# Performance work log

Hardware: AMD Instinct MI355X
Metric: run time of the kernel (lower is better)

Reference implementation:

```python
import jax, jax.numpy as jnp
import numpy as np

H = 16
D_IN = 1024
D_OUT = 1024
D_K = D_OUT // H
B = 8
S = 1024


def setup_inputs() -> dict:
    key = jax.random.key(0)
    ks = jax.random.split(key, 9)
    scale = 1.0 / np.sqrt(D_IN)
    inp = {
        "query": jax.random.normal(ks[0], (B, S, D_IN), dtype=jnp.float32),
        "key_": jax.random.normal(ks[1], (B, S, D_IN), dtype=jnp.float32),
        "value": jax.random.normal(ks[2], (B, S, D_IN), dtype=jnp.float32),
        "Wq": jax.random.uniform(ks[3], (D_OUT, D_IN), jnp.float32, -scale, scale),
        "bq": jax.random.uniform(ks[4], (D_OUT,), jnp.float32, -scale, scale),
        "Wk": jax.random.uniform(ks[5], (D_OUT, D_IN), jnp.float32, -scale, scale),
        "bk": jax.random.uniform(ks[6], (D_OUT,), jnp.float32, -scale, scale),
        "Wv": jax.random.uniform(ks[7], (D_OUT, D_IN), jnp.float32, -scale, scale),
        "bv": jax.random.uniform(ks[8], (D_OUT,), jnp.float32, -scale, scale),
    }
    return inp


def reference(query, key_, value, Wq, bq, Wk, bk, Wv, bv):
    batch = query.shape[0]

    def proj(x, W, b):
        # torch Linear: x @ W.T + b, then view(B, -1, h, d_k).transpose(1, 2)
        y = jnp.einsum("bsd,od->bso", x, W) + b
        return y.reshape(batch, -1, H, D_K).transpose(0, 2, 1, 3)  # [B, h, S, d_k]

    q = proj(query, Wq, bq)
    k = proj(key_, Wk, bk)
    v = proj(value, Wv, bv)

    scores = jnp.einsum("bhqd,bhkd->bhqk", q, k) / (D_K ** 0.5)  # [B, h, S, S]
    attn = jax.nn.softmax(scores, axis=-1)
    x = jnp.einsum("bhqk,bhkd->bhqd", attn, v)  # [B, h, S, d_k]

    # transpose(1, 2).contiguous().view(batch, -1) -> flatten seq*d_out
    return x.transpose(0, 2, 1, 3).reshape(batch, -1)
```

## Files before the change

### kernel.cpp

```cpp
#include <hip/hip_runtime.h>
#include <math.h>

#define NH   16
#define DK   64
#define SEQL 1024
#define NB   8
#define DIN  1024
#define PSTR 76

typedef __bf16 bf16;
typedef __attribute__((ext_vector_type(8))) __bf16 bf16x8;
typedef __attribute__((ext_vector_type(4))) __bf16 bf16x4;
typedef __attribute__((ext_vector_type(4))) float f32x4;

#define QSCALE 0.18033688011112042f

static __device__ __forceinline__ f32x4 mfma_bf16(bf16x8 a, bf16x8 b, f32x4 c) {
  return __builtin_amdgcn_mfma_f32_16x16x32_bf16(a, b, c, 0, 0, 0);
}

static __device__ __forceinline__ void async16(const bf16* g, bf16* l) {
  __builtin_amdgcn_global_load_lds(
      (const __attribute__((address_space(1))) void*)g,
      (__attribute__((address_space(3))) void*)l, 16, 0, 0);
}

__global__ __launch_bounds__(256)
void cvt6_kernel(const float* __restrict__ s0, const float* __restrict__ s1,
                 const float* __restrict__ s2, const float* __restrict__ s3,
                 const float* __restrict__ s4, const float* __restrict__ s5,
                 bf16* __restrict__ d0, bf16* __restrict__ d1,
                 bf16* __restrict__ d2, bf16* __restrict__ d3,
                 bf16* __restrict__ d4, bf16* __restrict__ d5,
                 int n8a, int n8b) {
  const int y = blockIdx.y;
  const int n8 = (y < 3) ? n8a : n8b;
  const int i = blockIdx.x * 256 + threadIdx.x;
  if (i >= n8) return;
  const float* s = (y == 0) ? s0 : (y == 1) ? s1 : (y == 2) ? s2
                 : (y == 3) ? s3 : (y == 4) ? s4 : s5;
  bf16* d = (y == 0) ? d0 : (y == 1) ? d1 : (y == 2) ? d2
          : (y == 3) ? d3 : (y == 4) ? d4 : d5;
  const f32x4* sp = (const f32x4*)s;
  const f32x4 a = sp[2 * i], b = sp[2 * i + 1];
  bf16x8 r;
  r[0] = (bf16)a[0]; r[1] = (bf16)a[1]; r[2] = (bf16)a[2]; r[3] = (bf16)a[3];
  r[4] = (bf16)b[0]; r[5] = (bf16)b[1]; r[6] = (bf16)b[2]; r[7] = (bf16)b[3];
  ((bf16x8*)d)[i] = r;
}

__global__ __launch_bounds__(256, 2)
void proj_kernel(const bf16* __restrict__ Xq, const bf16* __restrict__ Xk,
                 const bf16* __restrict__ Xv,
                 const bf16* __restrict__ Wq, const bf16* __restrict__ Wk,
                 const bf16* __restrict__ Wv,
                 const float* __restrict__ Bq, const float* __restrict__ Bk,
                 const float* __restrict__ Bv,
                 bf16* __restrict__ Yq, bf16* __restrict__ Yk,
                 bf16* __restrict__ Yv) {
  const int z = blockIdx.z;
  const bf16*  X  = (z == 0) ? Xq : (z == 1) ? Xk : Xv;
  const bf16*  W  = (z == 0) ? Wq : (z == 1) ? Wk : Wv;
  const float* Bi = (z == 0) ? Bq : (z == 1) ? Bk : Bv;
  bf16*        Y  = (z == 0) ? Yq : (z == 1) ? Yk : Yv;

  const int m0 = blockIdx.x * 128;
  const int n0 = blockIdx.y * 128;

  __shared__ __attribute__((aligned(16))) bf16 As[128 * 32];
  __shared__ __attribute__((aligned(16))) bf16 Bs[128 * 32];

  const int t    = threadIdx.x;
  const int l    = t & 63;
  const int w    = t >> 6;
  const int l15  = l & 15;
  const int quad = l >> 4;
  const int wm   = w & 1;
  const int wn   = w >> 1;

  f32x4 acc[4][4];
#pragma unroll
  for (int i = 0; i < 4; ++i)
#pragma unroll
    for (int j = 0; j < 4; ++j) acc[i][j] = (f32x4){0.f, 0.f, 0.f, 0.f};

  const int srow   = l >> 2;
  const int gchunk = (l & 3) ^ ((l >> 3) & 3);

  for (int k0 = 0; k0 < DIN; k0 += 32) {
    __syncthreads();
#pragma unroll
    for (int i = 0; i < 2; ++i) {
      const int slab = w * 32 + i * 16;
      const int r    = slab + srow;
      async16(X + (size_t)(m0 + r) * DIN + k0 + gchunk * 8, As + slab * 32);
      async16(W + (size_t)(n0 + r) * DIN + k0 + gchunk * 8, Bs + slab * 32);
    }
    __syncthreads();

    bf16x8 af[4], bfr[4];
    const int swz = quad ^ ((l15 >> 1) & 3);
#pragma unroll
    for (int mi = 0; mi < 4; ++mi)
      af[mi] = *(const bf16x8*)(As + (wm * 64 + mi * 16 + l15) * 32 + swz * 8);
#pragma unroll
    for (int nj = 0; nj < 4; ++nj)
      bfr[nj] = *(const bf16x8*)(Bs + (wn * 64 + nj * 16 + l15) * 32 + swz * 8);
#pragma unroll
    for (int mi = 0; mi < 4; ++mi)
#pragma unroll
      for (int nj = 0; nj < 4; ++nj)
        acc[mi][nj] = mfma_bf16(af[mi], bfr[nj], acc[mi][nj]);
  }

  if (z == 2) {
#pragma unroll
    for (int nj = 0; nj < 4; ++nj) {
      const int o    = n0 + wn * 64 + nj * 16 + l15;
      const float bv = Bi[o];
      const int h    = o >> 6;
      const int d    = o & 63;
#pragma unroll
      for (int mi = 0; mi < 4; ++mi) {
        const int m  = m0 + wm * 64 + mi * 16 + quad * 4;
        const int bl = m >> 10;
        const int s  = m & (SEQL - 1);
        bf16x4 pk;
#pragma unroll
        for (int r = 0; r < 4; ++r) pk[r] = (bf16)(acc[mi][nj][r] + bv);
        *(bf16x4*)(Y + ((size_t)(bl * NH + h) * DK + d) * SEQL + s) = pk;
      }
    }
  } else {
    const float scale = (z == 0) ? QSCALE : 1.0f;
#pragma unroll
    for (int nj = 0; nj < 4; ++nj) {
      const int o    = n0 + wn * 64 + nj * 16 + l15;
      const float bv = Bi[o];
      const int h    = o >> 6;
      const int d    = o & 63;
#pragma unroll
      for (int mi = 0; mi < 4; ++mi) {
#pragma unroll
        for (int r = 0; r < 4; ++r) {
          const int m  = m0 + wm * 64 + mi * 16 + quad * 4 + r;
          const int bl = m >> 10;
          const int s  = m & (SEQL - 1);
          Y[(size_t)(((bl * NH + h) << 10) | s) * DK + d] =
              (bf16)((acc[mi][nj][r] + bv) * scale);
        }
      }
    }
  }
}

__global__ __launch_bounds__(256, 2)
void attn_kernel(const bf16* __restrict__ Q, const bf16* __restrict__ K,
                 const bf16* __restrict__ V, float* __restrict__ Out, int b0) {
  const int bhl = blockIdx.x;
  const int q0  = blockIdx.y * 256;
  const int bg  = b0 + (bhl >> 4);
  const int h   = bhl & 15;
  const int t    = threadIdx.x;
  const int l    = t & 63;
  const int w    = t >> 6;
  const int l15  = l & 15;
  const int quad = l >> 4;

  const bf16* Qh = Q + (size_t)bhl * SEQL * DK;
  const bf16* Kh = K + (size_t)bhl * SEQL * DK;
  const bf16* Vh = V + (size_t)bhl * DK * SEQL;

  __shared__ __attribute__((aligned(16))) bf16 sKs[2][64 * 64];
  __shared__ __attribute__((aligned(16))) bf16 sVt[2][64 * 64];
  __shared__ __attribute__((aligned(16))) bf16 sPl[4][4][16 * PSTR];

  bf16x8 qf[4][2];
#pragma unroll
  for (int g = 0; g < 4; ++g)
#pragma unroll
    for (int hh = 0; hh < 2; ++hh)
      qf[g][hh] = *(const bf16x8*)(Qh + (size_t)(q0 + w * 64 + g * 16 + l15) * DK +
                                   hh * 32 + quad * 8);

  bf16x8 ones;
#pragma unroll
  for (int j = 0; j < 8; ++j) ones[j] = (bf16)1.0f;

  f32x4 oacc[4][4];
#pragma unroll
  for (int g = 0; g < 4; ++g)
#pragma unroll
    for (int n = 0; n < 4; ++n) oacc[g][n] = (f32x4){0.f, 0.f, 0.f, 0.f};
  f32x4 sacc[4];
#pragma unroll
  for (int g = 0; g < 4; ++g) sacc[g] = (f32x4){0.f, 0.f, 0.f, 0.f};

  const int drow   = l >> 3;
  const int dchunk = l & 7;

#define STAGE_KV(T, BB)                                                      \
  {                                                                          \
    const int kbs = (T) * 64;                                                \
    _Pragma("unroll")                                                        \
    for (int i = 0; i < 2; ++i) {                                            \
      const int r = w * 16 + i * 8 + drow;                                   \
      async16(Kh + (size_t)(kbs + r) * DK + (dchunk ^ (r & 7)) * 8,          \
              &sKs[BB][(w * 16 + i * 8) * 64]);                              \
      async16(Vh + (size_t)r * SEQL + kbs + (dchunk ^ (r & 7)) * 8,          \
              &sVt[BB][(w * 16 + i * 8) * 64]);                              \
    }                                                                        \
  }

  const int NT = SEQL / 64;

  STAGE_KV(0, 0)
  STAGE_KV(1, 1)
  asm volatile("s_waitcnt vmcnt(4)" ::: "memory");
  __builtin_amdgcn_s_barrier();

  for (int tt = 0; tt < NT; ++tt) {
    const int bb = tt & 1;

    bf16x8 kf[4][2];
#pragma unroll
    for (int c = 0; c < 4; ++c)
#pragma unroll
      for (int hh = 0; hh < 2; ++hh)
        kf[c][hh] = *(const bf16x8*)(&sKs[bb][(c * 16 + l15) * 64 +
                                     (((hh * 4 + quad) ^ (l15 & 7)) * 8)]);
    bf16x8 vfr[4][2];
#pragma unroll
    for (int n = 0; n < 4; ++n)
#pragma unroll
      for (int hh = 0; hh < 2; ++hh)
        vfr[n][hh] = *(const bf16x8*)(&sVt[bb][(n * 16 + l15) * 64 +
                                      (((hh * 4 + quad) ^ (l15 & 7)) * 8)]);

    asm volatile("s_waitcnt lgkmcnt(0)" ::: "memory");
    __builtin_amdgcn_sched_barrier(0);
    __builtin_amdgcn_s_barrier();
    if (tt + 2 < NT) STAGE_KV(tt + 2, bb)
    __builtin_amdgcn_sched_barrier(0);

#pragma unroll
    for (int g = 0; g < 4; ++g) {
#pragma unroll
      for (int c = 0; c < 4; ++c) {
        f32x4 cs = (f32x4){0.f, 0.f, 0.f, 0.f};
        cs = mfma_bf16(kf[c][0], qf[g][0], cs);
        cs = mfma_bf16(kf[c][1], qf[g][1], cs);
        bf16x4 pk;
#pragma unroll
        for (int r = 0; r < 4; ++r) pk[r] = (bf16)exp2f(cs[r]);
        *(bf16x4*)(&sPl[w][g][l15 * PSTR + c * 16 + quad * 4]) = pk;
      }
    }

#pragma unroll
    for (int g = 0; g < 4; ++g) {
      const bf16x8 pf0 = *(const bf16x8*)(&sPl[w][g][l15 * PSTR + quad * 8]);
      const bf16x8 pf1 = *(const bf16x8*)(&sPl[w][g][l15 * PSTR + 32 + quad * 8]);
#pragma unroll
      for (int n = 0; n < 4; ++n) {
        oacc[g][n] = mfma_bf16(pf0, vfr[n][0], oacc[g][n]);
        oacc[g][n] = mfma_bf16(pf1, vfr[n][1], oacc[g][n]);
      }
      sacc[g] = mfma_bf16(pf0, ones, sacc[g]);
      sacc[g] = mfma_bf16(pf1, ones, sacc[g]);
    }

    if (tt + 2 < NT) {
      asm volatile("s_waitcnt vmcnt(4)" ::: "memory");
    } else if (tt + 2 == NT) {
      asm volatile("s_waitcnt vmcnt(0)" ::: "memory");
    }
    if (tt + 1 < NT) __builtin_amdgcn_s_barrier();
  }
#undef STAGE_KV

#pragma unroll
  for (int g = 0; g < 4; ++g) {
    float linv[4];
#pragma unroll
    for (int r = 0; r < 4; ++r) linv[r] = 1.0f / sacc[g][r];
#pragma unroll
    for (int n = 0; n < 4; ++n) {
      const int d = n * 16 + l15;
#pragma unroll
      for (int r = 0; r < 4; ++r) {
        const int qrow = q0 + w * 64 + g * 16 + quad * 4 + r;
        Out[(size_t)((bg * SEQL + qrow) * NH + h) * DK + d] =
            oacc[g][n][r] * linv[r];
      }
    }
  }
}

extern "C" void kernel_launch(void* const* d_in, const int* in_sizes, int n_in,
                              void* d_out, int out_size, void* d_ws,
                              size_t ws_size, hipStream_t stream) {
  const float* q  = (const float*)d_in[0];
  const float* k  = (const float*)d_in[1];
  const float* v  = (const float*)d_in[2];
  const float* Wq = (const float*)d_in[3];
  const float* bq = (const float*)d_in[4];
  const float* Wk = (const float*)d_in[5];
  const float* bk = (const float*)d_in[6];
  const float* Wv = (const float*)d_in[7];
  const float* bv = (const float*)d_in[8];
  float* out = (float*)d_out;

  const size_t wElems = (size_t)DIN * DIN;
  const size_t wBytes = 3 * wElems * sizeof(bf16);
  const size_t perBatch = 6 * (size_t)SEQL * DIN * sizeof(bf16);
  int nbg = (ws_size > wBytes) ? (int)((ws_size - wBytes) / perBatch) : 1;
  if (nbg < 1) nbg = 1;
  if (nbg > NB) nbg = NB;

  bf16* Wqb = (bf16*)d_ws;
  bf16* Wkb = Wqb + wElems;
  bf16* Wvb = Wkb + wElems;
  const size_t g1 = (size_t)nbg * SEQL * DIN;
  bf16* Xqb = Wvb + wElems;
  bf16* Xkb = Xqb + g1;
  bf16* Xvb = Xkb + g1;
  bf16* Yqb = Xvb + g1;
  bf16* Ykb = Yqb + g1;
  bf16* Yvb = Ykb + g1;

  const int w8 = (int)(wElems / 8);

  for (int b0 = 0; b0 < NB; b0 += nbg) {
    const int nb = (NB - b0 < nbg) ? (NB - b0) : nbg;
    const int n8 = nb * SEQL * DIN / 8;
    const size_t xoff = (size_t)b0 * SEQL * DIN;
    const int xb = (n8 + 255) / 256;
    const int wb = (w8 + 255) / 256;
    dim3 gX((xb > wb) ? xb : wb, 6);
    cvt6_kernel<<<gX, 256, 0, stream>>>(q + xoff, k + xoff, v + xoff,
                                        Wq, Wk, Wv,
                                        Xqb, Xkb, Xvb, Wqb, Wkb, Wvb,
                                        n8, w8);

    dim3 gP(nb * 8, 8, 3);
    proj_kernel<<<gP, 256, 0, stream>>>(Xqb, Xkb, Xvb, Wqb, Wkb, Wvb,
                                        bq, bk, bv, Yqb, Ykb, Yvb);

    dim3 gA(nb * NH, SEQL / 256);
    attn_kernel<<<gA, 256, 0, stream>>>(Yqb, Ykb, Yvb, out, b0);
  }
}
```

Measured before the change: 279.7 us.

## Halve attention query tile, raise occupancy, and vectorize Q/K projection stores

The attention kernel now gives each block 128 query rows instead of 256 (32 per wave). It launches twice as many blocks with a launch-bounds target of 4 blocks per CU. V fragments are read from LDS on demand, and the barrier plus next K/V prefetch move to the end of each iteration, which lowers register pressure but shortens the load/compute overlap. In the projection kernel, the Q/K paths swap MFMA operand roles so each lane holds contiguous d elements and can write bf16x4 vector stores instead of scattered scalar stores, at the cost of more K/V reloads per query.

```diff
diff --git a/kernel.cpp b/kernel.cpp
--- a/kernel.cpp
+++ b/kernel.cpp
@@ -78,6 +78,11 @@
   const int wm   = w & 1;
   const int wn   = w >> 1;
 
+  const bf16* Atile = (z == 2) ? As : Bs;
+  const bf16* Btile = (z == 2) ? Bs : As;
+  const int arow0 = ((z == 2) ? wm : wn) * 64;
+  const int brow0 = ((z == 2) ? wn : wm) * 64;
+
   f32x4 acc[4][4];
 #pragma unroll
   for (int i = 0; i < 4; ++i)
@@ -102,10 +107,10 @@
     const int swz = quad ^ ((l15 >> 1) & 3);
 #pragma unroll
     for (int mi = 0; mi < 4; ++mi)
-      af[mi] = *(const bf16x8*)(As + (wm * 64 + mi * 16 + l15) * 32 + swz * 8);
+      af[mi] = *(const bf16x8*)(Atile + (arow0 + mi * 16 + l15) * 32 + swz * 8);
 #pragma unroll
     for (int nj = 0; nj < 4; ++nj)
-      bfr[nj] = *(const bf16x8*)(Bs + (wn * 64 + nj * 16 + l15) * 32 + swz * 8);
+      bfr[nj] = *(const bf16x8*)(Btile + (brow0 + nj * 16 + l15) * 32 + swz * 8);
 #pragma unroll
     for (int mi = 0; mi < 4; ++mi)
 #pragma unroll
@@ -133,32 +138,31 @@
     }
   } else {
     const float scale = (z == 0) ? QSCALE : 1.0f;
-#pragma unroll
-    for (int nj = 0; nj < 4; ++nj) {
-      const int o    = n0 + wn * 64 + nj * 16 + l15;
-      const float bv = Bi[o];
-      const int h    = o >> 6;
-      const int d    = o & 63;
-#pragma unroll
-      for (int mi = 0; mi < 4; ++mi) {
-#pragma unroll
-        for (int r = 0; r < 4; ++r) {
-          const int m  = m0 + wm * 64 + mi * 16 + quad * 4 + r;
-          const int bl = m >> 10;
-          const int s  = m & (SEQL - 1);
-          Y[(size_t)(((bl * NH + h) << 10) | s) * DK + d] =
-              (bf16)((acc[mi][nj][r] + bv) * scale);
-        }
-      }
-    }
-  }
-}
-
-__global__ __launch_bounds__(256, 2)
+    const int hq = (n0 + wn * 64) >> 6;
+#pragma unroll
+    for (int mi = 0; mi < 4; ++mi) {
+      const int dbase = mi * 16 + quad * 4;
+      const f32x4 bv4 = *(const f32x4*)(Bi + n0 + wn * 64 + dbase);
+#pragma unroll
+      for (int nj = 0; nj < 4; ++nj) {
+        const int m  = m0 + wm * 64 + nj * 16 + l15;
+        const int bl = m >> 10;
+        const int s  = m & (SEQL - 1);
+        bf16x4 pk;
+#pragma unroll
+        for (int r = 0; r < 4; ++r)
+          pk[r] = (bf16)((acc[mi][nj][r] + bv4[r]) * scale);
+        *(bf16x4*)(Y + (size_t)(((bl * NH + hq) << 10) | s) * DK + dbase) = pk;
+      }
+    }
+  }
+}
+
+__global__ __launch_bounds__(256, 4)
 void attn_kernel(const bf16* __restrict__ Q, const bf16* __restrict__ K,
                  const bf16* __restrict__ V, float* __restrict__ Out, int b0) {
   const int bhl = blockIdx.x;
-  const int q0  = blockIdx.y * 256;
+  const int q0  = blockIdx.y * 128;
   const int bg  = b0 + (bhl >> 4);
   const int h   = bhl & 15;
   const int t    = threadIdx.x;
@@ -173,28 +177,28 @@
 
   __shared__ __attribute__((aligned(16))) bf16 sKs[2][64 * 64];
   __shared__ __attribute__((aligned(16))) bf16 sVt[2][64 * 64];
-  __shared__ __attribute__((aligned(16))) bf16 sPl[4][4][16 * PSTR];
-
-  bf16x8 qf[4][2];
-#pragma unroll
-  for (int g = 0; g < 4; ++g)
+  __shared__ __attribute__((aligned(16))) bf16 sPl[4][2][16 * PSTR];
+
+  bf16x8 qf[2][2];
+#pragma unroll
+  for (int g = 0; g < 2; ++g)
 #pragma unroll
     for (int hh = 0; hh < 2; ++hh)
-      qf[g][hh] = *(const bf16x8*)(Qh + (size_t)(q0 + w * 64 + g * 16 + l15) * DK +
+      qf[g][hh] = *(const bf16x8*)(Qh + (size_t)(q0 + w * 32 + g * 16 + l15) * DK +
                                    hh * 32 + quad * 8);
 
   bf16x8 ones;
 #pragma unroll
   for (int j = 0; j < 8; ++j) ones[j] = (bf16)1.0f;
 
-  f32x4 oacc[4][4];
-#pragma unroll
-  for (int g = 0; g < 4; ++g)
+  f32x4 oacc[2][4];
+#pragma unroll
+  for (int g = 0; g < 2; ++g)
 #pragma unroll
     for (int n = 0; n < 4; ++n) oacc[g][n] = (f32x4){0.f, 0.f, 0.f, 0.f};
-  f32x4 sacc[4];
-#pragma unroll
-  for (int g = 0; g < 4; ++g) sacc[g] = (f32x4){0.f, 0.f, 0.f, 0.f};
+  f32x4 sacc[2];
+  sacc[0] = (f32x4){0.f, 0.f, 0.f, 0.f};
+  sacc[1] = (f32x4){0.f, 0.f, 0.f, 0.f};
 
   const int drow   = l >> 3;
   const int dchunk = l & 7;
@@ -229,22 +233,9 @@
       for (int hh = 0; hh < 2; ++hh)
         kf[c][hh] = *(const bf16x8*)(&sKs[bb][(c * 16 + l15) * 64 +
                                      (((hh * 4 + quad) ^ (l15 & 7)) * 8)]);
-    bf16x8 vfr[4][2];
-#pragma unroll
-    for (int n = 0; n < 4; ++n)
-#pragma unroll
-      for (int hh = 0; hh < 2; ++hh)
-        vfr[n][hh] = *(const bf16x8*)(&sVt[bb][(n * 16 + l15) * 64 +
-                                      (((hh * 4 + quad) ^ (l15 & 7)) * 8)]);
-
-    asm volatile("s_waitcnt lgkmcnt(0)" ::: "memory");
-    __builtin_amdgcn_sched_barrier(0);
-    __builtin_amdgcn_s_barrier();
-    if (tt + 2 < NT) STAGE_KV(tt + 2, bb)
-    __builtin_amdgcn_sched_barrier(0);
-
-#pragma unroll
-    for (int g = 0; g < 4; ++g) {
+
+#pragma unroll
+    for (int g = 0; g < 2; ++g) {
 #pragma unroll
       for (int c = 0; c < 4; ++c) {
         f32x4 cs = (f32x4){0.f, 0.f, 0.f, 0.f};
@@ -257,20 +248,36 @@
       }
     }
 
-#pragma unroll
-    for (int g = 0; g < 4; ++g) {
-      const bf16x8 pf0 = *(const bf16x8*)(&sPl[w][g][l15 * PSTR + quad * 8]);
-      const bf16x8 pf1 = *(const bf16x8*)(&sPl[w][g][l15 * PSTR + 32 + quad * 8]);
-#pragma unroll
-      for (int n = 0; n < 4; ++n) {
-        oacc[g][n] = mfma_bf16(pf0, vfr[n][0], oacc[g][n]);
-        oacc[g][n] = mfma_bf16(pf1, vfr[n][1], oacc[g][n]);
-      }
-      sacc[g] = mfma_bf16(pf0, ones, sacc[g]);
-      sacc[g] = mfma_bf16(pf1, ones, sacc[g]);
-    }
-
+    bf16x8 pf[2][2];
+#pragma unroll
+    for (int g = 0; g < 2; ++g) {
+      pf[g][0] = *(const bf16x8*)(&sPl[w][g][l15 * PSTR + quad * 8]);
+      pf[g][1] = *(const bf16x8*)(&sPl[w][g][l15 * PSTR + 32 + quad * 8]);
+    }
+
+#pragma unroll
+    for (int n = 0; n < 4; ++n) {
+      const bf16x8 v0 = *(const bf16x8*)(&sVt[bb][(n * 16 + l15) * 64 +
+                                         ((quad ^ (l15 & 7)) * 8)]);
+      const bf16x8 v1 = *(const bf16x8*)(&sVt[bb][(n * 16 + l15) * 64 +
+                                         ((((4 + quad)) ^ (l15 & 7)) * 8)]);
+#pragma unroll
+      for (int g = 0; g < 2; ++g) {
+        oacc[g][n] = mfma_bf16(pf[g][0], v0, oacc[g][n]);
+        oacc[g][n] = mfma_bf16(pf[g][1], v1, oacc[g][n]);
+      }
+    }
+#pragma unroll
+    for (int g = 0; g < 2; ++g) {
+      sacc[g] = mfma_bf16(pf[g][0], ones, sacc[g]);
+      sacc[g] = mfma_bf16(pf[g][1], ones, sacc[g]);
+    }
+
+    asm volatile("s_waitcnt lgkmcnt(0)" ::: "memory");
+    __builtin_amdgcn_sched_barrier(0);
+    __builtin_amdgcn_s_barrier();
     if (tt + 2 < NT) {
+      STAGE_KV(tt + 2, bb)
       asm volatile("s_waitcnt vmcnt(4)" ::: "memory");
     } else if (tt + 2 == NT) {
       asm volatile("s_waitcnt vmcnt(0)" ::: "memory");
@@ -280,7 +287,7 @@
 #undef STAGE_KV
 
 #pragma unroll
-  for (int g = 0; g < 4; ++g) {
+  for (int g = 0; g < 2; ++g) {
     float linv[4];
 #pragma unroll
     for (int r = 0; r < 4; ++r) linv[r] = 1.0f / sacc[g][r];
@@ -289,7 +296,7 @@
       const int d = n * 16 + l15;
 #pragma unroll
       for (int r = 0; r < 4; ++r) {
-        const int qrow = q0 + w * 64 + g * 16 + quad * 4 + r;
+        const int qrow = q0 + w * 32 + g * 16 + quad * 4 + r;
         Out[(size_t)((bg * SEQL + qrow) * NH + h) * DK + d] =
             oacc[g][n][r] * linv[r];
       }
@@ -347,7 +354,7 @@
     proj_kernel<<<gP, 256, 0, stream>>>(Xqb, Xkb, Xvb, Wqb, Wkb, Wvb,
                                         bq, bk, bv, Yqb, Ykb, Yvb);
 
-    dim3 gA(nb * NH, SEQL / 256);
+    dim3 gA(nb * NH, SEQL / 128);
     attn_kernel<<<gA, 256, 0, stream>>>(Yqb, Ykb, Yvb, out, b0);
   }
 }
```

After: 293.2 us. 4.8% more time.

## Fuse activation fp32-to-bf16 conversion into projection GEMM loads

Applied to the files above, without the earlier changes.

Instead of a separate pass that converts query/key/value to bf16 in the workspace, the projection kernel now loads fp32 activations straight into shared memory with async loads and converts to bf16 while reading fragments. Only the weights are still pre-converted, in a single kernel outside the batch loop. For Q and K the MFMA operand order is swapped, so the epilogue writes contiguous bf16x4 vectors along d with vectorised bias loads instead of scalar scattered stores. This removes an extra round trip of activations through global memory, but doubles shared memory for the X tile and adds conversion work inside the GEMM loop.

```diff
diff --git a/kernel.cpp b/kernel.cpp
--- a/kernel.cpp
+++ b/kernel.cpp
@@ -19,28 +19,20 @@
   return __builtin_amdgcn_mfma_f32_16x16x32_bf16(a, b, c, 0, 0, 0);
 }
 
-static __device__ __forceinline__ void async16(const bf16* g, bf16* l) {
+static __device__ __forceinline__ void async16(const void* g, void* l) {
   __builtin_amdgcn_global_load_lds(
       (const __attribute__((address_space(1))) void*)g,
       (__attribute__((address_space(3))) void*)l, 16, 0, 0);
 }
 
 __global__ __launch_bounds__(256)
-void cvt6_kernel(const float* __restrict__ s0, const float* __restrict__ s1,
-                 const float* __restrict__ s2, const float* __restrict__ s3,
-                 const float* __restrict__ s4, const float* __restrict__ s5,
-                 bf16* __restrict__ d0, bf16* __restrict__ d1,
-                 bf16* __restrict__ d2, bf16* __restrict__ d3,
-                 bf16* __restrict__ d4, bf16* __restrict__ d5,
-                 int n8a, int n8b) {
-  const int y = blockIdx.y;
-  const int n8 = (y < 3) ? n8a : n8b;
+void cvt3_kernel(const float* __restrict__ s0, const float* __restrict__ s1,
+                 const float* __restrict__ s2, bf16* __restrict__ d0,
+                 bf16* __restrict__ d1, bf16* __restrict__ d2, int n8) {
   const int i = blockIdx.x * 256 + threadIdx.x;
   if (i >= n8) return;
-  const float* s = (y == 0) ? s0 : (y == 1) ? s1 : (y == 2) ? s2
-                 : (y == 3) ? s3 : (y == 4) ? s4 : s5;
-  bf16* d = (y == 0) ? d0 : (y == 1) ? d1 : (y == 2) ? d2
-          : (y == 3) ? d3 : (y == 4) ? d4 : d5;
+  const float* s = (blockIdx.y == 0) ? s0 : (blockIdx.y == 1) ? s1 : s2;
+  bf16*        d = (blockIdx.y == 0) ? d0 : (blockIdx.y == 1) ? d1 : d2;
   const f32x4* sp = (const f32x4*)s;
   const f32x4 a = sp[2 * i], b = sp[2 * i + 1];
   bf16x8 r;
@@ -50,8 +42,8 @@
 }
 
 __global__ __launch_bounds__(256, 2)
-void proj_kernel(const bf16* __restrict__ Xq, const bf16* __restrict__ Xk,
-                 const bf16* __restrict__ Xv,
+void proj_kernel(const float* __restrict__ Xq, const float* __restrict__ Xk,
+                 const float* __restrict__ Xv,
                  const bf16* __restrict__ Wq, const bf16* __restrict__ Wk,
                  const bf16* __restrict__ Wv,
                  const float* __restrict__ Bq, const float* __restrict__ Bk,
@@ -59,7 +51,7 @@
                  bf16* __restrict__ Yq, bf16* __restrict__ Yk,
                  bf16* __restrict__ Yv) {
   const int z = blockIdx.z;
-  const bf16*  X  = (z == 0) ? Xq : (z == 1) ? Xk : Xv;
+  const float* X  = (z == 0) ? Xq : (z == 1) ? Xk : Xv;
   const bf16*  W  = (z == 0) ? Wq : (z == 1) ? Wk : Wv;
   const float* Bi = (z == 0) ? Bq : (z == 1) ? Bk : Bv;
   bf16*        Y  = (z == 0) ? Yq : (z == 1) ? Yk : Yv;
@@ -67,8 +59,8 @@
   const int m0 = blockIdx.x * 128;
   const int n0 = blockIdx.y * 128;
 
-  __shared__ __attribute__((aligned(16))) bf16 As[128 * 32];
-  __shared__ __attribute__((aligned(16))) bf16 Bs[128 * 32];
+  __shared__ __attribute__((aligned(16))) float Xs[128 * 32];
+  __shared__ __attribute__((aligned(16))) bf16  Ws[128 * 32];
 
   const int t    = threadIdx.x;
   const int l    = t & 63;
@@ -86,6 +78,10 @@
 
   const int srow   = l >> 2;
   const int gchunk = (l & 3) ^ ((l >> 3) & 3);
+  const int xrow   = l >> 3;
+  const int xchunk = (l & 7) ^ xrow;
+
+  const int rx7 = l15 & 7;
 
   for (int k0 = 0; k0 < DIN; k0 += 32) {
     __syncthreads();
@@ -93,24 +89,43 @@
     for (int i = 0; i < 2; ++i) {
       const int slab = w * 32 + i * 16;
       const int r    = slab + srow;
-      async16(X + (size_t)(m0 + r) * DIN + k0 + gchunk * 8, As + slab * 32);
-      async16(W + (size_t)(n0 + r) * DIN + k0 + gchunk * 8, Bs + slab * 32);
+      async16(W + (size_t)(n0 + r) * DIN + k0 + gchunk * 8, Ws + slab * 32);
+    }
+#pragma unroll
+    for (int c = 0; c < 4; ++c) {
+      const int slab = w * 32 + c * 8;
+      const int r    = slab + xrow;
+      async16(X + (size_t)(m0 + r) * DIN + k0 + xchunk * 4, Xs + slab * 32);
     }
     __syncthreads();
 
-    bf16x8 af[4], bfr[4];
-    const int swz = quad ^ ((l15 >> 1) & 3);
-#pragma unroll
-    for (int mi = 0; mi < 4; ++mi)
-      af[mi] = *(const bf16x8*)(As + (wm * 64 + mi * 16 + l15) * 32 + swz * 8);
-#pragma unroll
-    for (int nj = 0; nj < 4; ++nj)
-      bfr[nj] = *(const bf16x8*)(Bs + (wn * 64 + nj * 16 + l15) * 32 + swz * 8);
-#pragma unroll
-    for (int mi = 0; mi < 4; ++mi)
-#pragma unroll
-      for (int nj = 0; nj < 4; ++nj)
-        acc[mi][nj] = mfma_bf16(af[mi], bfr[nj], acc[mi][nj]);
+    bf16x8 xf[4], wf[4];
+    const int swzW = quad ^ ((l15 >> 1) & 3);
+#pragma unroll
+    for (int i = 0; i < 4; ++i) {
+      const int xr = wm * 64 + i * 16 + l15;
+      const f32x4 lo = *(const f32x4*)(Xs + xr * 32 + (((quad << 1) | 0) ^ rx7) * 4);
+      const f32x4 hi = *(const f32x4*)(Xs + xr * 32 + (((quad << 1) | 1) ^ rx7) * 4);
+#pragma unroll
+      for (int j = 0; j < 4; ++j) {
+        xf[i][j]     = (bf16)lo[j];
+        xf[i][4 + j] = (bf16)hi[j];
+      }
+      wf[i] = *(const bf16x8*)(Ws + (wn * 64 + i * 16 + l15) * 32 + swzW * 8);
+    }
+    if (z == 2) {
+#pragma unroll
+      for (int mi = 0; mi < 4; ++mi)
+#pragma unroll
+        for (int nj = 0; nj < 4; ++nj)
+          acc[mi][nj] = mfma_bf16(xf[mi], wf[nj], acc[mi][nj]);
+    } else {
+#pragma unroll
+      for (int mi = 0; mi < 4; ++mi)
+#pragma unroll
+        for (int nj = 0; nj < 4; ++nj)
+          acc[mi][nj] = mfma_bf16(wf[mi], xf[nj], acc[mi][nj]);
+    }
   }
 
   if (z == 2) {
@@ -133,22 +148,21 @@
     }
   } else {
     const float scale = (z == 0) ? QSCALE : 1.0f;
-#pragma unroll
-    for (int nj = 0; nj < 4; ++nj) {
-      const int o    = n0 + wn * 64 + nj * 16 + l15;
-      const float bv = Bi[o];
-      const int h    = o >> 6;
-      const int d    = o & 63;
-#pragma unroll
-      for (int mi = 0; mi < 4; ++mi) {
-#pragma unroll
-        for (int r = 0; r < 4; ++r) {
-          const int m  = m0 + wm * 64 + mi * 16 + quad * 4 + r;
-          const int bl = m >> 10;
-          const int s  = m & (SEQL - 1);
-          Y[(size_t)(((bl * NH + h) << 10) | s) * DK + d] =
-              (bf16)((acc[mi][nj][r] + bv) * scale);
-        }
+    const int hq = (n0 + wn * 64) >> 6;
+#pragma unroll
+    for (int mi = 0; mi < 4; ++mi) {
+      const int dbase = mi * 16 + quad * 4;
+      const f32x4 bv4 = *(const f32x4*)(Bi + n0 + wn * 64 + dbase);
+#pragma unroll
+      for (int nj = 0; nj < 4; ++nj) {
+        const int m  = m0 + wm * 64 + nj * 16 + l15;
+        const int bl = m >> 10;
+        const int s  = m & (SEQL - 1);
+        bf16x4 pk;
+#pragma unroll
+        for (int r = 0; r < 4; ++r)
+          pk[r] = (bf16)((acc[mi][nj][r] + bv4[r]) * scale);
+        *(bf16x4*)(Y + (size_t)(((bl * NH + hq) << 10) | s) * DK + dbase) = pk;
       }
     }
   }
@@ -313,7 +327,7 @@
 
   const size_t wElems = (size_t)DIN * DIN;
   const size_t wBytes = 3 * wElems * sizeof(bf16);
-  const size_t perBatch = 6 * (size_t)SEQL * DIN * sizeof(bf16);
+  const size_t perBatch = 3 * (size_t)SEQL * DIN * sizeof(bf16);
   int nbg = (ws_size > wBytes) ? (int)((ws_size - wBytes) / perBatch) : 1;
   if (nbg < 1) nbg = 1;
   if (nbg > NB) nbg = NB;
@@ -322,29 +336,21 @@
   bf16* Wkb = Wqb + wElems;
   bf16* Wvb = Wkb + wElems;
   const size_t g1 = (size_t)nbg * SEQL * DIN;
-  bf16* Xqb = Wvb + wElems;
-  bf16* Xkb = Xqb + g1;
-  bf16* Xvb = Xkb + g1;
-  bf16* Yqb = Xvb + g1;
+  bf16* Yqb = Wvb + wElems;
   bf16* Ykb = Yqb + g1;
   bf16* Yvb = Ykb + g1;
 
   const int w8 = (int)(wElems / 8);
+  dim3 gW((w8 + 255) / 256, 3);
+  cvt3_kernel<<<gW, 256, 0, stream>>>(Wq, Wk, Wv, Wqb, Wkb, Wvb, w8);
 
   for (int b0 = 0; b0 < NB; b0 += nbg) {
     const int nb = (NB - b0 < nbg) ? (NB - b0) : nbg;
-    const int n8 = nb * SEQL * DIN / 8;
     const size_t xoff = (size_t)b0 * SEQL * DIN;
-    const int xb = (n8 + 255) / 256;
-    const int wb = (w8 + 255) / 256;
-    dim3 gX((xb > wb) ? xb : wb, 6);
-    cvt6_kernel<<<gX, 256, 0, stream>>>(q + xoff, k + xoff, v + xoff,
-                                        Wq, Wk, Wv,
-                                        Xqb, Xkb, Xvb, Wqb, Wkb, Wvb,
-                                        n8, w8);
 
     dim3 gP(nb * 8, 8, 3);
-    proj_kernel<<<gP, 256, 0, stream>>>(Xqb, Xkb, Xvb, Wqb, Wkb, Wvb,
+    proj_kernel<<<gP, 256, 0, stream>>>(q + xoff, k + xoff, v + xoff,
+                                        Wqb, Wkb, Wvb,
                                         bq, bk, bv, Yqb, Ykb, Yvb);
 
     dim3 gA(nb * NH, SEQL / 256);
```

Result: slower. 316.3 us (+13.1%).

## Double projection K-tile to 64 and transpose MFMA operands for vectorized Q/K stores

Applied to the files above, without the earlier changes.

The projection GEMM now stages 64-wide K slices in LDS instead of 32, using an 8-chunk XOR swizzle. This halves the number of barrier pairs and loop iterations and issues two MFMAs per fragment pair. For the Q and K outputs, the MFMA operands are swapped so each lane holds four consecutive d values, which allows packed 8-byte bf16x4 stores with a vectorized bias load in place of scalar scattered 2-byte stores. LDS use per block doubles, which may affect occupancy.

```diff
diff --git a/kernel.cpp b/kernel.cpp
--- a/kernel.cpp
+++ b/kernel.cpp
@@ -19,7 +19,7 @@
   return __builtin_amdgcn_mfma_f32_16x16x32_bf16(a, b, c, 0, 0, 0);
 }
 
-static __device__ __forceinline__ void async16(const bf16* g, bf16* l) {
+static __device__ __forceinline__ void async16(const void* g, void* l) {
   __builtin_amdgcn_global_load_lds(
       (const __attribute__((address_space(1))) void*)g,
       (__attribute__((address_space(3))) void*)l, 16, 0, 0);
@@ -67,8 +67,8 @@
   const int m0 = blockIdx.x * 128;
   const int n0 = blockIdx.y * 128;
 
-  __shared__ __attribute__((aligned(16))) bf16 As[128 * 32];
-  __shared__ __attribute__((aligned(16))) bf16 Bs[128 * 32];
+  __shared__ __attribute__((aligned(16))) bf16 As[128 * 64];
+  __shared__ __attribute__((aligned(16))) bf16 Bs[128 * 64];
 
   const int t    = threadIdx.x;
   const int l    = t & 63;
@@ -84,33 +84,50 @@
 #pragma unroll
     for (int j = 0; j < 4; ++j) acc[i][j] = (f32x4){0.f, 0.f, 0.f, 0.f};
 
-  const int srow   = l >> 2;
-  const int gchunk = (l & 3) ^ ((l >> 3) & 3);
-
-  for (int k0 = 0; k0 < DIN; k0 += 32) {
+  const int srow = l >> 3;
+  const int gc8  = (l & 7) ^ srow;
+  const int rx7  = l15 & 7;
+
+  for (int k0 = 0; k0 < DIN; k0 += 64) {
     __syncthreads();
 #pragma unroll
-    for (int i = 0; i < 2; ++i) {
-      const int slab = w * 32 + i * 16;
+    for (int c = 0; c < 4; ++c) {
+      const int slab = w * 32 + c * 8;
       const int r    = slab + srow;
-      async16(X + (size_t)(m0 + r) * DIN + k0 + gchunk * 8, As + slab * 32);
-      async16(W + (size_t)(n0 + r) * DIN + k0 + gchunk * 8, Bs + slab * 32);
+      async16(X + (size_t)(m0 + r) * DIN + k0 + gc8 * 8, As + slab * 64);
+      async16(W + (size_t)(n0 + r) * DIN + k0 + gc8 * 8, Bs + slab * 64);
     }
     __syncthreads();
 
-    bf16x8 af[4], bfr[4];
-    const int swz = quad ^ ((l15 >> 1) & 3);
-#pragma unroll
-    for (int mi = 0; mi < 4; ++mi)
-      af[mi] = *(const bf16x8*)(As + (wm * 64 + mi * 16 + l15) * 32 + swz * 8);
-#pragma unroll
-    for (int nj = 0; nj < 4; ++nj)
-      bfr[nj] = *(const bf16x8*)(Bs + (wn * 64 + nj * 16 + l15) * 32 + swz * 8);
-#pragma unroll
-    for (int mi = 0; mi < 4; ++mi)
-#pragma unroll
-      for (int nj = 0; nj < 4; ++nj)
-        acc[mi][nj] = mfma_bf16(af[mi], bfr[nj], acc[mi][nj]);
+    bf16x8 xf[4][2], wf[4][2];
+#pragma unroll
+    for (int i = 0; i < 4; ++i) {
+      const int xr = wm * 64 + i * 16 + l15;
+      const int wr = wn * 64 + i * 16 + l15;
+#pragma unroll
+      for (int hh = 0; hh < 2; ++hh) {
+        const int chs = ((hh * 4 + quad) ^ rx7) * 8;
+        xf[i][hh] = *(const bf16x8*)(As + xr * 64 + chs);
+        wf[i][hh] = *(const bf16x8*)(Bs + wr * 64 + chs);
+      }
+    }
+    if (z == 2) {
+#pragma unroll
+      for (int mi = 0; mi < 4; ++mi)
+#pragma unroll
+        for (int nj = 0; nj < 4; ++nj) {
+          acc[mi][nj] = mfma_bf16(xf[mi][0], wf[nj][0], acc[mi][nj]);
+          acc[mi][nj] = mfma_bf16(xf[mi][1], wf[nj][1], acc[mi][nj]);
+        }
+    } else {
+#pragma unroll
+      for (int mi = 0; mi < 4; ++mi)
+#pragma unroll
+        for (int nj = 0; nj < 4; ++nj) {
+          acc[mi][nj] = mfma_bf16(wf[mi][0], xf[nj][0], acc[mi][nj]);
+          acc[mi][nj] = mfma_bf16(wf[mi][1], xf[nj][1], acc[mi][nj]);
+        }
+    }
   }
 
   if (z == 2) {
@@ -133,22 +150,21 @@
     }
   } else {
     const float scale = (z == 0) ? QSCALE : 1.0f;
-#pragma unroll
-    for (int nj = 0; nj < 4; ++nj) {
-      const int o    = n0 + wn * 64 + nj * 16 + l15;
-      const float bv = Bi[o];
-      const int h    = o >> 6;
-      const int d    = o & 63;
-#pragma unroll
-      for (int mi = 0; mi < 4; ++mi) {
-#pragma unroll
-        for (int r = 0; r < 4; ++r) {
-          const int m  = m0 + wm * 64 + mi * 16 + quad * 4 + r;
-          const int bl = m >> 10;
-          const int s  = m & (SEQL - 1);
-          Y[(size_t)(((bl * NH + h) << 10) | s) * DK + d] =
-              (bf16)((acc[mi][nj][r] + bv) * scale);
-        }
+    const int hq = (n0 + wn * 64) >> 6;
+#pragma unroll
+    for (int mi = 0; mi < 4; ++mi) {
+      const int dbase = mi * 16 + quad * 4;
+      const f32x4 bv4 = *(const f32x4*)(Bi + n0 + wn * 64 + dbase);
+#pragma unroll
+      for (int nj = 0; nj < 4; ++nj) {
+        const int m  = m0 + wm * 64 + nj * 16 + l15;
+        const int bl = m >> 10;
+        const int s  = m & (SEQL - 1);
+        bf16x4 pk;
+#pragma unroll
+        for (int r = 0; r < 4; ++r)
+          pk[r] = (bf16)((acc[mi][nj][r] + bv4[r]) * scale);
+        *(bf16x4*)(Y + (size_t)(((bl * NH + hq) << 10) | s) * DK + dbase) = pk;
       }
     }
   }
```

New measurement: 276.4 us. About the same (-1.2%).
